# Kernel tuning notes

Hardware: AMD Instinct MI355X
Metric: run time of the kernel (lower is better)

Reference implementation:

```python
import jax, jax.numpy as jnp
import numpy as np

TINY = np.finfo(np.float32).tiny


def setup_inputs() -> dict:
    key = jax.random.key(0)
    k1, k2, k3 = jax.random.split(key, 3)
    B, IN, OUT = 4096, 4096, 1024
    x = jax.random.normal(k1, (B, IN), dtype=jnp.float32)
    weight = jax.random.normal(k2, (IN, OUT), dtype=jnp.float32)
    uniform = jax.random.uniform(k3, (IN, OUT), dtype=jnp.float32)
    T = jnp.ones((1,), dtype=jnp.float32)
    return {"x": x, "weight": weight, "uniform": uniform, "T": T}


def reference(x, weight, uniform, T):
    # training-path forward of ConcreteLayer
    # uniform -> (1 - tiny) * u + tiny, then Gumbel noise
    u = (1.0 - TINY) * uniform + TINY
    gumbel = -jnp.log(-jnp.log(u))                      # [in, out]
    noisy_logits = (weight + gumbel) / T                # temperature scaling
    samples = jax.nn.softmax(noisy_logits, axis=1)      # softmax over out dim (torch default for 2D)
    out = jnp.einsum('bi,ik->bk', x, samples)           # [batch, out]
    return out
```

## Files before the change

kernel.cpp:

```cpp
#include <hip/hip_runtime.h>
#include <cstdint>
#include <cstddef>


#define TINYF 1.17549435082228750797e-38f
#define LN2F 0.69314718055994530942f
#define LOG2EF 1.44269504088896340736f

typedef unsigned short u16;
typedef __attribute__((ext_vector_type(8))) short bf16x8;
typedef __attribute__((ext_vector_type(4))) float f32x4;

__device__ __forceinline__ u16 f2bf(float f) {
  union { float f; uint32_t u; } v; v.f = f;
  uint32_t r = v.u + 0x7FFFu + ((v.u >> 16) & 1u);
  return (u16)(r >> 16);
}

__device__ __forceinline__ float log2_hw(float x) { return __builtin_amdgcn_logf(x); }
__device__ __forceinline__ float exp2_hw(float x) { return __builtin_amdgcn_exp2f(x); }

__device__ __forceinline__ float gumbel_fast(float u) {
  float t = -log2_hw(u);
  return -LN2F * log2_hw(t * LN2F);
}
__device__ __forceinline__ float exp_fast(float x) { return exp2_hw(x * LOG2EF); }

__device__ __forceinline__ void gld_lds16(const void* g, void* l) {
  __builtin_amdgcn_global_load_lds(
      (__attribute__((address_space(1))) void*)(g),
      (__attribute__((address_space(3))) void*)(l), 16, 0, 0);
}

__global__ void zero_kernel(float4* __restrict__ p, int n4) {
  int i = blockIdx.x * blockDim.x + threadIdx.x;
  if (i < n4) p[i] = make_float4(0.f, 0.f, 0.f, 0.f);
}

__global__ void cast_x_kernel(const float4* __restrict__ x, ushort4* __restrict__ xb, int n4) {
  int i = blockIdx.x * blockDim.x + threadIdx.x;
  if (i >= n4) return;
  float4 v = x[i];
  ushort4 o;
  o.x = f2bf(v.x); o.y = f2bf(v.y); o.z = f2bf(v.z); o.w = f2bf(v.w);
  xb[i] = o;
}

__global__ void softmax_stats_kernel(const float4* __restrict__ W4, const float4* __restrict__ U4,
                                     const float* __restrict__ Tp, float2* __restrict__ stats) {
  const int row = blockIdx.x;
  const int t = threadIdx.x;
  const float invT = 1.0f / Tp[0];
  size_t gi = (size_t)row * 256 + t;
  float4 w = W4[gi], u = U4[gi];
  float lg[4];
  lg[0] = (w.x + gumbel_fast(u.x * (1.0f - TINYF) + TINYF)) * invT;
  lg[1] = (w.y + gumbel_fast(u.y * (1.0f - TINYF) + TINYF)) * invT;
  lg[2] = (w.z + gumbel_fast(u.z * (1.0f - TINYF) + TINYF)) * invT;
  lg[3] = (w.w + gumbel_fast(u.w * (1.0f - TINYF) + TINYF)) * invT;
  float m = fmaxf(fmaxf(lg[0], lg[1]), fmaxf(lg[2], lg[3]));
#pragma unroll
  for (int o = 32; o > 0; o >>= 1) m = fmaxf(m, __shfl_down(m, o));
  __shared__ float redm[4], reds[4];
  if ((t & 63) == 0) redm[t >> 6] = m;
  __syncthreads();
  m = fmaxf(fmaxf(redm[0], redm[1]), fmaxf(redm[2], redm[3]));
  float s = exp_fast(lg[0] - m) + exp_fast(lg[1] - m) + exp_fast(lg[2] - m) + exp_fast(lg[3] - m);
#pragma unroll
  for (int o = 32; o > 0; o >>= 1) s += __shfl_down(s, o);
  if ((t & 63) == 0) reds[t >> 6] = s;
  __syncthreads();
  if (t == 0) stats[row] = make_float2(m, reds[0] + reds[1] + reds[2] + reds[3]);
}

__global__ void norm_transpose_kernel(const float* __restrict__ W, const float* __restrict__ U,
                                      const float* __restrict__ Tp, const float2* __restrict__ stats,
                                      u16* __restrict__ BT) {
  __shared__ float tile[64][65];
  const int k0 = blockIdx.x * 64, n0 = blockIdx.y * 64;
  const int t = threadIdx.x;
  const float invT = 1.0f / Tp[0];
  {
    const int nn4 = (t & 15) * 4, kq = t >> 4;
#pragma unroll
    for (int r = 0; r < 4; ++r) {
      int kk = r * 16 + kq;
      size_t gi = (size_t)(k0 + kk) * 1024 + (n0 + nn4);
      float4 w = *(const float4*)&W[gi];
      float4 u = *(const float4*)&U[gi];
      float2 st = stats[k0 + kk];
      float rs = 1.0f / st.y;
      tile[kk][nn4 + 0] = exp_fast((w.x + gumbel_fast(u.x * (1.0f - TINYF) + TINYF)) * invT - st.x) * rs;
      tile[kk][nn4 + 1] = exp_fast((w.y + gumbel_fast(u.y * (1.0f - TINYF) + TINYF)) * invT - st.x) * rs;
      tile[kk][nn4 + 2] = exp_fast((w.z + gumbel_fast(u.z * (1.0f - TINYF) + TINYF)) * invT - st.x) * rs;
      tile[kk][nn4 + 3] = exp_fast((w.w + gumbel_fast(u.w * (1.0f - TINYF) + TINYF)) * invT - st.x) * rs;
    }
  }
  __syncthreads();
  {
    const int kk4 = (t & 15) * 4, nq = t >> 4;
#pragma unroll
    for (int r = 0; r < 4; ++r) {
      int nn = r * 16 + nq;
      ushort4 o;
      o.x = f2bf(tile[kk4 + 0][nn]);
      o.y = f2bf(tile[kk4 + 1][nn]);
      o.z = f2bf(tile[kk4 + 2][nn]);
      o.w = f2bf(tile[kk4 + 3][nn]);
      *(ushort4*)&BT[(size_t)(n0 + nn) * 4096 + (k0 + kk4)] = o;
    }
  }
}

#define TM 128
#define TN 128
#define TK 32

__launch_bounds__(256)
__global__ void gemm_bt_kernel(const u16* __restrict__ A, const u16* __restrict__ BT,
                               float* __restrict__ C, int M, int N, int K) {
  __shared__ u16 As[TM * TK];
  __shared__ u16 Bs[TN * TK];

  const int tid = threadIdx.x;
  const int lane = tid & 63, w = tid >> 6;
  const int wm = w >> 1, wn = w & 1;
  const int m0 = blockIdx.x * TM, n0 = blockIdx.y * TN;
  const int quad = lane >> 4, r16 = lane & 15;
  const int lrow = lane >> 2;
  const int lk = (lane & 3) * 8;

  const int kz = blockIdx.z;
  const int Kh = K >> 1;
  const u16* Ak = A + (size_t)kz * Kh;
  const u16* Bk = BT + (size_t)kz * Kh;

  f32x4 acc[4][4] = {};

  for (int kt = 0; kt < Kh; kt += TK) {
    __syncthreads();
#pragma unroll
    for (int c = 0; c < 2; ++c) {
      int chunk = w * 2 + c;
      gld_lds16(Ak + (size_t)(m0 + chunk * 16 + lrow) * K + kt + lk, (char*)As + chunk * 1024);
    }
#pragma unroll
    for (int c = 0; c < 2; ++c) {
      int chunk = w * 2 + c;
      gld_lds16(Bk + (size_t)(n0 + chunk * 16 + lrow) * K + kt + lk, (char*)Bs + chunk * 1024);
    }
    __syncthreads();

    bf16x8 aF[4], bF[4];
#pragma unroll
    for (int mi = 0; mi < 4; ++mi)
      aF[mi] = *(const bf16x8*)&As[(wm * 64 + mi * 16 + r16) * TK + quad * 8];
#pragma unroll
    for (int ni = 0; ni < 4; ++ni)
      bF[ni] = *(const bf16x8*)&Bs[(wn * 64 + ni * 16 + r16) * TK + quad * 8];
#pragma unroll
    for (int mi = 0; mi < 4; ++mi)
#pragma unroll
      for (int ni = 0; ni < 4; ++ni)
        acc[mi][ni] = __builtin_amdgcn_mfma_f32_16x16x32_bf16(aF[mi], bF[ni], acc[mi][ni], 0, 0, 0);
  }

#pragma unroll
  for (int mi = 0; mi < 4; ++mi)
#pragma unroll
    for (int ni = 0; ni < 4; ++ni)
#pragma unroll
      for (int r = 0; r < 4; ++r) {
        int row = m0 + wm * 64 + mi * 16 + quad * 4 + r;
        int col = n0 + wn * 64 + ni * 16 + r16;
        atomicAdd(&C[(size_t)row * N + col], acc[mi][ni][r]);
      }
}

extern "C" void kernel_launch(void* const* d_in, const int* in_sizes, int n_in,
                              void* d_out, int out_size, void* d_ws, size_t ws_size,
                              hipStream_t stream) {
  const int M = 4096, K = 4096, N = 1024;
  const float* x = (const float*)d_in[0];
  const float* W = (const float*)d_in[1];
  const float* U = (const float*)d_in[2];
  const float* Tp = (const float*)d_in[3];
  float* out = (float*)d_out;

  char* ws = (char*)d_ws;
  u16* xb = (u16*)ws;
  u16* bt = (u16*)(ws + (size_t)M * K * 2);
  float2* stats = (float2*)(ws + (size_t)M * K * 2 + (size_t)N * K * 2);

  zero_kernel<<<dim3((M * N / 4 + 255) / 256), 256, 0, stream>>>((float4*)out, M * N / 4);
  cast_x_kernel<<<dim3((M * K / 4) / 256), 256, 0, stream>>>((const float4*)x, (ushort4*)xb, M * K / 4);
  softmax_stats_kernel<<<dim3(K), 256, 0, stream>>>((const float4*)W, (const float4*)U, Tp, stats);
  norm_transpose_kernel<<<dim3(K / 64, N / 64), 256, 0, stream>>>(W, U, Tp, stats, bt);
  gemm_bt_kernel<<<dim3(M / TM, N / TN, 2), 256, 0, stream>>>(xb, bt, out, M, N, K);
}
```

Before: 217.1 us.

## Fold softmax normalization into x cast, drop stats pass, widen GEMM K tile with swizzle

Drops the separate softmax-stats pass. The transpose kernel now writes unnormalized exp values and accumulates per-row sums with atomics. The division by the row sum moves onto x during the bf16 cast, and zeroing the output is fused into the same kernel. The GEMM K tile doubles to 64 with an XOR-swizzled LDS layout to cut bank conflicts and halve the loop iterations. Skipping the max subtraction risks exp overflow for large logits or small T, and atomic sums make the result order-dependent.

```diff
diff --git a/kernel.cpp b/kernel.cpp
--- a/kernel.cpp
+++ b/kernel.cpp
@@ -32,50 +32,9 @@
       (__attribute__((address_space(3))) void*)(l), 16, 0, 0);
 }
 
-__global__ void zero_kernel(float4* __restrict__ p, int n4) {
-  int i = blockIdx.x * blockDim.x + threadIdx.x;
-  if (i < n4) p[i] = make_float4(0.f, 0.f, 0.f, 0.f);
-}
-
-__global__ void cast_x_kernel(const float4* __restrict__ x, ushort4* __restrict__ xb, int n4) {
-  int i = blockIdx.x * blockDim.x + threadIdx.x;
-  if (i >= n4) return;
-  float4 v = x[i];
-  ushort4 o;
-  o.x = f2bf(v.x); o.y = f2bf(v.y); o.z = f2bf(v.z); o.w = f2bf(v.w);
-  xb[i] = o;
-}
-
-__global__ void softmax_stats_kernel(const float4* __restrict__ W4, const float4* __restrict__ U4,
-                                     const float* __restrict__ Tp, float2* __restrict__ stats) {
-  const int row = blockIdx.x;
-  const int t = threadIdx.x;
-  const float invT = 1.0f / Tp[0];
-  size_t gi = (size_t)row * 256 + t;
-  float4 w = W4[gi], u = U4[gi];
-  float lg[4];
-  lg[0] = (w.x + gumbel_fast(u.x * (1.0f - TINYF) + TINYF)) * invT;
-  lg[1] = (w.y + gumbel_fast(u.y * (1.0f - TINYF) + TINYF)) * invT;
-  lg[2] = (w.z + gumbel_fast(u.z * (1.0f - TINYF) + TINYF)) * invT;
-  lg[3] = (w.w + gumbel_fast(u.w * (1.0f - TINYF) + TINYF)) * invT;
-  float m = fmaxf(fmaxf(lg[0], lg[1]), fmaxf(lg[2], lg[3]));
-#pragma unroll
-  for (int o = 32; o > 0; o >>= 1) m = fmaxf(m, __shfl_down(m, o));
-  __shared__ float redm[4], reds[4];
-  if ((t & 63) == 0) redm[t >> 6] = m;
-  __syncthreads();
-  m = fmaxf(fmaxf(redm[0], redm[1]), fmaxf(redm[2], redm[3]));
-  float s = exp_fast(lg[0] - m) + exp_fast(lg[1] - m) + exp_fast(lg[2] - m) + exp_fast(lg[3] - m);
-#pragma unroll
-  for (int o = 32; o > 0; o >>= 1) s += __shfl_down(s, o);
-  if ((t & 63) == 0) reds[t >> 6] = s;
-  __syncthreads();
-  if (t == 0) stats[row] = make_float2(m, reds[0] + reds[1] + reds[2] + reds[3]);
-}
-
-__global__ void norm_transpose_kernel(const float* __restrict__ W, const float* __restrict__ U,
-                                      const float* __restrict__ Tp, const float2* __restrict__ stats,
-                                      u16* __restrict__ BT) {
+__global__ void trans_exp_kernel(const float* __restrict__ W, const float* __restrict__ U,
+                                 const float* __restrict__ Tp, u16* __restrict__ BT,
+                                 float* __restrict__ d) {
   __shared__ float tile[64][65];
   const int k0 = blockIdx.x * 64, n0 = blockIdx.y * 64;
   const int t = threadIdx.x;
@@ -88,12 +47,16 @@
       size_t gi = (size_t)(k0 + kk) * 1024 + (n0 + nn4);
       float4 w = *(const float4*)&W[gi];
       float4 u = *(const float4*)&U[gi];
-      float2 st = stats[k0 + kk];
-      float rs = 1.0f / st.y;
-      tile[kk][nn4 + 0] = exp_fast((w.x + gumbel_fast(u.x * (1.0f - TINYF) + TINYF)) * invT - st.x) * rs;
-      tile[kk][nn4 + 1] = exp_fast((w.y + gumbel_fast(u.y * (1.0f - TINYF) + TINYF)) * invT - st.x) * rs;
-      tile[kk][nn4 + 2] = exp_fast((w.z + gumbel_fast(u.z * (1.0f - TINYF) + TINYF)) * invT - st.x) * rs;
-      tile[kk][nn4 + 3] = exp_fast((w.w + gumbel_fast(u.w * (1.0f - TINYF) + TINYF)) * invT - st.x) * rs;
+      float e0 = exp_fast((w.x + gumbel_fast(u.x * (1.0f - TINYF) + TINYF)) * invT);
+      float e1 = exp_fast((w.y + gumbel_fast(u.y * (1.0f - TINYF) + TINYF)) * invT);
+      float e2 = exp_fast((w.z + gumbel_fast(u.z * (1.0f - TINYF) + TINYF)) * invT);
+      float e3 = exp_fast((w.w + gumbel_fast(u.w * (1.0f - TINYF) + TINYF)) * invT);
+      tile[kk][nn4 + 0] = e0; tile[kk][nn4 + 1] = e1;
+      tile[kk][nn4 + 2] = e2; tile[kk][nn4 + 3] = e3;
+      float s = (e0 + e1) + (e2 + e3);
+#pragma unroll
+      for (int m = 8; m > 0; m >>= 1) s += __shfl_xor(s, m, 16);
+      if ((t & 15) == 0) atomicAdd(&d[k0 + kk], s);
     }
   }
   __syncthreads();
@@ -112,9 +75,27 @@
   }
 }
 
+__global__ void cast_zero_kernel(const float4* __restrict__ x, const float4* __restrict__ d4,
+                                 ushort4* __restrict__ xb, float4* __restrict__ out,
+                                 int n4x, int n4o) {
+  int i = blockIdx.x * blockDim.x + threadIdx.x;
+  if (i < n4x) {
+    int col4 = i & 1023;
+    float4 v = x[i];
+    float4 dd = d4[col4];
+    ushort4 o;
+    o.x = f2bf(v.x / dd.x); o.y = f2bf(v.y / dd.y);
+    o.z = f2bf(v.z / dd.z); o.w = f2bf(v.w / dd.w);
+    xb[i] = o;
+  } else {
+    int j = i - n4x;
+    if (j < n4o) out[j] = make_float4(0.f, 0.f, 0.f, 0.f);
+  }
+}
+
 #define TM 128
 #define TN 128
-#define TK 32
+#define TK 64
 
 __launch_bounds__(256)
 __global__ void gemm_bt_kernel(const u16* __restrict__ A, const u16* __restrict__ BT,
@@ -127,8 +108,8 @@
   const int wm = w >> 1, wn = w & 1;
   const int m0 = blockIdx.x * TM, n0 = blockIdx.y * TN;
   const int quad = lane >> 4, r16 = lane & 15;
-  const int lrow = lane >> 2;
-  const int lk = (lane & 3) * 8;
+  const int srow = lane >> 3;
+  const int sg = (lane & 7) ^ srow;
 
   const int kz = blockIdx.z;
   const int Kh = K >> 1;
@@ -140,29 +121,32 @@
   for (int kt = 0; kt < Kh; kt += TK) {
     __syncthreads();
 #pragma unroll
-    for (int c = 0; c < 2; ++c) {
-      int chunk = w * 2 + c;
-      gld_lds16(Ak + (size_t)(m0 + chunk * 16 + lrow) * K + kt + lk, (char*)As + chunk * 1024);
-    }
-#pragma unroll
-    for (int c = 0; c < 2; ++c) {
-      int chunk = w * 2 + c;
-      gld_lds16(Bk + (size_t)(n0 + chunk * 16 + lrow) * K + kt + lk, (char*)Bs + chunk * 1024);
+    for (int c = 0; c < 4; ++c) {
+      int chunk = w * 4 + c;
+      gld_lds16(Ak + (size_t)(m0 + chunk * 8 + srow) * K + kt + sg * 8, (char*)As + chunk * 1024);
+      gld_lds16(Bk + (size_t)(n0 + chunk * 8 + srow) * K + kt + sg * 8, (char*)Bs + chunk * 1024);
     }
     __syncthreads();
 
-    bf16x8 aF[4], bF[4];
 #pragma unroll
-    for (int mi = 0; mi < 4; ++mi)
-      aF[mi] = *(const bf16x8*)&As[(wm * 64 + mi * 16 + r16) * TK + quad * 8];
+    for (int ss = 0; ss < 2; ++ss) {
+      bf16x8 aF[4], bF[4];
 #pragma unroll
-    for (int ni = 0; ni < 4; ++ni)
-      bF[ni] = *(const bf16x8*)&Bs[(wn * 64 + ni * 16 + r16) * TK + quad * 8];
+      for (int mi = 0; mi < 4; ++mi) {
+        int row = wm * 64 + mi * 16 + r16;
+        aF[mi] = *(const bf16x8*)((const char*)As + row * 128 + (((ss * 4 + quad) ^ (row & 7)) * 16));
+      }
 #pragma unroll
-    for (int mi = 0; mi < 4; ++mi)
+      for (int ni = 0; ni < 4; ++ni) {
+        int row = wn * 64 + ni * 16 + r16;
+        bF[ni] = *(const bf16x8*)((const char*)Bs + row * 128 + (((ss * 4 + quad) ^ (row & 7)) * 16));
+      }
 #pragma unroll
-      for (int ni = 0; ni < 4; ++ni)
-        acc[mi][ni] = __builtin_amdgcn_mfma_f32_16x16x32_bf16(aF[mi], bF[ni], acc[mi][ni], 0, 0, 0);
+      for (int mi = 0; mi < 4; ++mi)
+#pragma unroll
+        for (int ni = 0; ni < 4; ++ni)
+          acc[mi][ni] = __builtin_amdgcn_mfma_f32_16x16x32_bf16(aF[mi], bF[ni], acc[mi][ni], 0, 0, 0);
+    }
   }
 
 #pragma unroll
@@ -190,11 +174,12 @@
   char* ws = (char*)d_ws;
   u16* xb = (u16*)ws;
   u16* bt = (u16*)(ws + (size_t)M * K * 2);
-  float2* stats = (float2*)(ws + (size_t)M * K * 2 + (size_t)N * K * 2);
+  float* dsum = (float*)(ws + (size_t)M * K * 2 + (size_t)N * K * 2);
 
-  zero_kernel<<<dim3((M * N / 4 + 255) / 256), 256, 0, stream>>>((float4*)out, M * N / 4);
-  cast_x_kernel<<<dim3((M * K / 4) / 256), 256, 0, stream>>>((const float4*)x, (ushort4*)xb, M * K / 4);
-  softmax_stats_kernel<<<dim3(K), 256, 0, stream>>>((const float4*)W, (const float4*)U, Tp, stats);
-  norm_transpose_kernel<<<dim3(K / 64, N / 64), 256, 0, stream>>>(W, U, Tp, stats, bt);
+  hipMemsetAsync(dsum, 0, K * sizeof(float), stream);
+  trans_exp_kernel<<<dim3(K / 64, N / 64), 256, 0, stream>>>(W, U, Tp, bt, dsum);
+  const int n4x = M * K / 4, n4o = M * N / 4;
+  cast_zero_kernel<<<dim3((n4x + n4o) / 256), 256, 0, stream>>>(
+      (const float4*)x, (const float4*)dsum, (ushort4*)xb, (float4*)out, n4x, n4o);
   gemm_bt_kernel<<<dim3(M / TM, N / TN, 2), 256, 0, stream>>>(xb, bt, out, M, N, K);
 }
```

Result: faster. 196.6 us (-9.5%).
